# Performance work log

Measured on AMD Instinct MI355X. Metric: run time of the kernel, lower is better.

Reference implementation:

```python
import jax, jax.numpy as jnp
import numpy as np

H = 10                 # heads in both convs
EPS = 1e-5             # GraphNorm eps
N, E, D_NODE, D_EDGE, G = 100000, 1600000, 128, 32, 64


def _lin(key, out_d, in_d, bias=True):
    k1, k2 = jax.random.split(key)
    W = jax.random.normal(k1, (out_d, in_d), jnp.float32) / np.sqrt(in_d)
    if bias:
        b = jax.random.normal(k2, (out_d,), jnp.float32) * 0.01
        return W, b
    return W


def setup_inputs() -> dict:
    key = jax.random.key(0)
    ks = jax.random.split(key, 20)
    x = jax.random.normal(ks[0], (N, D_NODE), jnp.float32)
    edge_attr = jax.random.normal(ks[1], (E, D_EDGE), jnp.float32)
    edge_index = jax.random.randint(ks[2], (2, E), 0, N)
    batch_idx = jnp.sort(jax.random.randint(ks[3], (N,), 0, G))
    # conv1: in=128, out=5, heads=10
    q1W, q1b = _lin(ks[4], H * 5, D_NODE)
    k1W, k1b = _lin(ks[5], H * 5, D_NODE)
    v1W, v1b = _lin(ks[6], H * 5, D_NODE)
    e1W = _lin(ks[7], H * 5, D_EDGE, bias=False)
    s1W, s1b = _lin(ks[8], 5, D_NODE)        # lin_skip
    b1W = _lin(ks[9], 1, 3 * 5, bias=False)  # lin_beta
    # GraphNorm(5)
    gnW = jnp.ones((5,), jnp.float32)
    gnb = jnp.zeros((5,), jnp.float32)
    gnms = jnp.ones((5,), jnp.float32)       # mean_scale
    # conv2: in=5, out=1, heads=10
    q2W, q2b = _lin(ks[10], H * 1, 5)
    k2W, k2b = _lin(ks[11], H * 1, 5)
    v2W, v2b = _lin(ks[12], H * 1, 5)
    e2W = _lin(ks[13], H * 1, D_EDGE, bias=False)
    s2W, s2b = _lin(ks[14], 1, 5)
    b2W = _lin(ks[15], 1, 3 * 1, bias=False)
    return dict(x=x, edge_attr=edge_attr, edge_index=edge_index, batch_idx=batch_idx,
                q1W=q1W, q1b=q1b, k1W=k1W, k1b=k1b, v1W=v1W, v1b=v1b, e1W=e1W,
                s1W=s1W, s1b=s1b, b1W=b1W, gnW=gnW, gnb=gnb, gnms=gnms,
                q2W=q2W, q2b=q2b, k2W=k2W, k2b=k2b, v2W=v2W, v2b=v2b, e2W=e2W,
                s2W=s2W, s2b=s2b, b2W=b2W)


def _tconv(x, src, dst, edge_attr, qW, qb, kW, kb, vW, vb, eW, sW, sb, bW, c):
    """PyG TransformerConv: concat=False, beta=True, eval (dropout off)."""
    n = x.shape[0]
    q = (x @ qW.T + qb).reshape(n, H, c)
    k = (x @ kW.T + kb).reshape(n, H, c)
    v = (x @ vW.T + vb).reshape(n, H, c)
    e = (edge_attr @ eW.T).reshape(-1, H, c)            # [E,H,c]
    kj = k[src] + e                                      # gather + edge bias
    alpha = jnp.einsum('ehc,ehc->eh', q[dst], kj) / np.sqrt(c)
    amax = jax.lax.stop_gradient(jax.ops.segment_max(alpha, dst, num_segments=n))
    ex = jnp.exp(alpha - amax[dst])
    denom = jax.ops.segment_sum(ex, dst, num_segments=n)
    a = ex / denom[dst]                                  # segment softmax [E,H]
    out = jax.ops.segment_sum((v[src] + e) * a[:, :, None], dst, num_segments=n)
    out = out.mean(axis=1)                               # concat=False -> head mean [N,c]
    xr = x @ sW.T + sb                                   # skip
    beta = jax.nn.sigmoid(jnp.concatenate([out, xr, out - xr], -1) @ bW.T)
    return beta * xr + (1.0 - beta) * out


def _graph_norm(x, batch, w, b, ms):
    cnt = jnp.maximum(jax.ops.segment_sum(jnp.ones((x.shape[0],), x.dtype), batch,
                                          num_segments=G), 1.0)[:, None]
    mean = jax.ops.segment_sum(x, batch, num_segments=G) / cnt
    out = x - mean[batch] * ms
    var = jax.ops.segment_sum(out * out, batch, num_segments=G) / cnt
    return w * out / jnp.sqrt(var + EPS)[batch] + b


def reference(x, edge_attr, edge_index, batch_idx,
              q1W, q1b, k1W, k1b, v1W, v1b, e1W, s1W, s1b, b1W,
              gnW, gnb, gnms,
              q2W, q2b, k2W, k2b, v2W, v2b, e2W, s2W, s2b, b2W):
    src, dst = edge_index[0], edge_index[1]
    h = _tconv(x, src, dst, edge_attr, q1W, q1b, k1W, k1b, v1W, v1b, e1W,
               s1W, s1b, b1W, 5)
    h = jax.nn.relu(_graph_norm(h, batch_idx, gnW, gnb, gnms))
    out = _tconv(h, src, dst, edge_attr, q2W, q2b, k2W, k2b, v2W, v2b, e2W,
                 s2W, s2b, b2W, 1)
    return jax.nn.sigmoid(out)
```

## Files before the change

### kernel.cpp

```cpp
#include <hip/hip_runtime.h>
#include <math.h>


#define EPS 1e-5f
#define INV_SQRT5 0.44721359549995794f

__device__ __forceinline__ float f16_to_f32(unsigned short u) {
  union { unsigned short us; _Float16 h; } cv; cv.us = u;
  return (float)cv.h;
}

__device__ __forceinline__ void store40(const float (&acc)[40], int n, int g,
                                        float* __restrict__ q1, float* __restrict__ kv1,
                                        float* __restrict__ xr1) {
#pragma unroll
  for (int c = 0; c < 40; ++c) {
    int ch = g * 40 + c;
    if (ch < 50)        q1[(size_t)n * 52 + ch] = acc[c];
    else if (ch < 100)  kv1[(size_t)n * 104 + 2 * (ch - 50)] = acc[c];
    else if (ch < 150)  kv1[(size_t)n * 104 + 2 * (ch - 100) + 1] = acc[c];
    else if (ch < 155)  xr1[(size_t)n * 8 + (ch - 150)] = acc[c];
  }
}

__global__ __launch_bounds__(256, 4) void k_qkvs1(
    const float* __restrict__ x,
    const float* __restrict__ qW, const float* __restrict__ qb,
    const float* __restrict__ kW, const float* __restrict__ kb,
    const float* __restrict__ vW, const float* __restrict__ vb,
    const float* __restrict__ sW, const float* __restrict__ sb,
    float* __restrict__ q1, float* __restrict__ kv1,
    float* __restrict__ xr1, int n_nodes) {
  __shared__ __align__(16) float sWt[40 * 128];
  __shared__ float sB[40];
  const int t = threadIdx.x;
  const int g = blockIdx.y;
  const int n0 = blockIdx.x * 512;

  for (int i = t; i < 1280; i += 256) {
    int c = i >> 5, q = i & 31;
    int ch = g * 40 + c;
    float4 w = make_float4(0.f, 0.f, 0.f, 0.f);
    const float* srcr = nullptr;
    if (ch < 50)        srcr = qW + ch * 128;
    else if (ch < 100)  srcr = kW + (ch - 50) * 128;
    else if (ch < 150)  srcr = vW + (ch - 100) * 128;
    else if (ch < 155)  srcr = sW + (ch - 150) * 128;
    if (srcr) w = *(const float4*)(srcr + q * 4);
    *(float4*)&sWt[c * 128 + q * 4] = w;
  }
  if (t < 40) {
    int ch = g * 40 + t;
    float b = 0.f;
    if (ch < 50) b = qb[ch];
    else if (ch < 100) b = kb[ch - 50];
    else if (ch < 150) b = vb[ch - 100];
    else if (ch < 155) b = sb[ch - 150];
    sB[t] = b;
  }
  __syncthreads();

  float accA[40], accB[40];
#pragma unroll
  for (int c = 0; c < 40; ++c) { accA[c] = sB[c]; accB[c] = sB[c]; }
  const int na = n0 + 2 * t, nb = na + 1;
  const bool okA = na < n_nodes, okB = nb < n_nodes;
  const float* xa_p = x + (size_t)(okA ? na : 0) * 128;
  const float* xb_p = x + (size_t)(okB ? nb : 0) * 128;
  const float4* w4 = (const float4*)sWt;

  for (int kc = 0; kc < 128; kc += 8) {
    float4 xa0 = *(const float4*)(xa_p + kc);
    float4 xa1 = *(const float4*)(xa_p + kc + 4);
    float4 xb0 = *(const float4*)(xb_p + kc);
    float4 xb1 = *(const float4*)(xb_p + kc + 4);
    const int base = kc >> 2;
#pragma unroll
    for (int c = 0; c < 40; ++c) {
      float4 w0 = w4[c * 32 + base];
      float4 w1 = w4[c * 32 + base + 1];
      accA[c] = fmaf(w0.x, xa0.x, accA[c]); accA[c] = fmaf(w0.y, xa0.y, accA[c]);
      accA[c] = fmaf(w0.z, xa0.z, accA[c]); accA[c] = fmaf(w0.w, xa0.w, accA[c]);
      accA[c] = fmaf(w1.x, xa1.x, accA[c]); accA[c] = fmaf(w1.y, xa1.y, accA[c]);
      accA[c] = fmaf(w1.z, xa1.z, accA[c]); accA[c] = fmaf(w1.w, xa1.w, accA[c]);
      accB[c] = fmaf(w0.x, xb0.x, accB[c]); accB[c] = fmaf(w0.y, xb0.y, accB[c]);
      accB[c] = fmaf(w0.z, xb0.z, accB[c]); accB[c] = fmaf(w0.w, xb0.w, accB[c]);
      accB[c] = fmaf(w1.x, xb1.x, accB[c]); accB[c] = fmaf(w1.y, xb1.y, accB[c]);
      accB[c] = fmaf(w1.z, xb1.z, accB[c]); accB[c] = fmaf(w1.w, xb1.w, accB[c]);
    }
  }
  if (okA) store40(accA, na, g, q1, kv1, xr1);
  if (okB) store40(accB, nb, g, q1, kv1, xr1);
}

__global__ __launch_bounds__(256) void k_hist(const int* __restrict__ ei, int n_edges,
                                              int* __restrict__ cnt) {
  int e = blockIdx.x * 256 + threadIdx.x;
  if (e < n_edges) atomicAdd(&cnt[ei[n_edges + e]], 1);
}

__global__ __launch_bounds__(1024) void k_scan(const int* __restrict__ cnt,
                                               int* __restrict__ rp,
                                               int* __restrict__ cursor, int n) {
  __shared__ int ls[1024];
  int tid = threadIdx.x;
  const int CH = (((n + 1023) / 1024) + 3) & ~3;
  int lo = tid * CH, hi = min(lo + CH, n);
  int s = 0;
  if (lo < n) {
    int full = (hi - lo) & ~3;
    const int4* c4 = (const int4*)(cnt + lo);
    for (int i = 0; i < full; i += 4) {
      int4 v = c4[i >> 2];
      s += v.x + v.y + v.z + v.w;
    }
    for (int i = lo + full; i < hi; ++i) s += cnt[i];
  }
  ls[tid] = s;
  __syncthreads();
  for (int off = 1; off < 1024; off <<= 1) {
    int v = (tid >= off) ? ls[tid - off] : 0;
    __syncthreads();
    ls[tid] += v;
    __syncthreads();
  }
  int run = (tid > 0) ? ls[tid - 1] : 0;
  for (int i = lo; i < hi; ++i) {
    rp[i] = run; cursor[i] = run; run += cnt[i];
  }
  if (hi == n && lo < n) rp[n] = run;
}

__global__ __launch_bounds__(256) void k_scatter(const int* __restrict__ ei, int n_edges,
                                                 int* __restrict__ cursor,
                                                 int* __restrict__ seid,
                                                 int* __restrict__ ssrc) {
  int e = blockIdx.x * 256 + threadIdx.x;
  if (e >= n_edges) return;
  int s = ei[e];
  int d = ei[n_edges + e];
  int p = atomicAdd(&cursor[d], 1);
  seid[p] = e;
  ssrc[p] = s;
}

__global__ __launch_bounds__(256) void k_evt(
    float* attr, const float* __restrict__ e1W, const float* __restrict__ e2W,
    int n_edges) {
  int e = blockIdx.x * 256 + threadIdx.x;
  if (e >= n_edges) return;
  const float4* ar = (const float4*)(attr + (size_t)e * 32);
  float4 a[8];
#pragma unroll
  for (int j = 0; j < 8; ++j) a[j] = ar[j];
  unsigned int d[30];
#pragma unroll
  for (int c2 = 0; c2 < 30; ++c2) {
    int c0 = 2 * c2, c1 = 2 * c2 + 1;
    const float* w0 = (c0 < 50) ? (e1W + c0 * 32) : (e2W + (c0 - 50) * 32);
    const float* w1 = (c1 < 50) ? (e1W + c1 * 32) : (e2W + (c1 - 50) * 32);
    float acc0 = 0.f, acc1 = 0.f;
#pragma unroll
    for (int j = 0; j < 8; ++j) {
      float4 wa = *(const float4*)(w0 + 4 * j);
      float4 wb = *(const float4*)(w1 + 4 * j);
      acc0 = fmaf(wa.x, a[j].x, acc0); acc0 = fmaf(wa.y, a[j].y, acc0);
      acc0 = fmaf(wa.z, a[j].z, acc0); acc0 = fmaf(wa.w, a[j].w, acc0);
      acc1 = fmaf(wb.x, a[j].x, acc1); acc1 = fmaf(wb.y, a[j].y, acc1);
      acc1 = fmaf(wb.z, a[j].z, acc1); acc1 = fmaf(wb.w, a[j].w, acc1);
    }
    union { _Float16 h[2]; unsigned int u; } p;
    p.h[0] = (_Float16)acc0; p.h[1] = (_Float16)acc1;
    d[c2] = p.u;
  }
  unsigned int* row = (unsigned int*)(attr + (size_t)e * 32);
#pragma unroll
  for (int k = 0; k < 7; ++k)
    *(uint4*)(row + 4 * k) = make_uint4(d[4 * k], d[4 * k + 1], d[4 * k + 2], d[4 * k + 3]);
  *(uint2*)(row + 28) = make_uint2(d[28], d[29]);
}

__global__ __launch_bounds__(256) void k_conv1(
    const int* __restrict__ rp, const int* __restrict__ seid,
    const int* __restrict__ ssrc, const float* __restrict__ attr,
    const float* __restrict__ q1, const float* __restrict__ kv1,
    const float* __restrict__ xr1,
    const float* __restrict__ bW, float* __restrict__ h1, int n_nodes) {
  const int lane = threadIdx.x & 63;
  const int wid = (blockIdx.x * 256 + threadIdx.x) >> 6;
  const int nw = gridDim.x * 4;
  const int wr = (lane < 50) ? lane : 0;
  const int g0 = (wr / 5) * 5;
  const int cp = lane % 5;
  const unsigned short* evr = (const unsigned short*)attr;

  for (int n = wid; n < n_nodes; n += nw) {
    const int p0 = rp[n], deg = rp[n + 1] - p0;
    const float qc = q1[(size_t)n * 52 + wr];
    int eL = 0, sL = 0;
    if (lane < deg) { eL = seid[p0 + lane]; sL = ssrc[p0 + lane]; }
    float accN0 = 0.f, accD0 = 0.f, accN1 = 0.f, accD1 = 0.f;
    int i = 0;
    for (; i + 2 <= deg; i += 2) {
      int e0, s0, e1, s1;
      if (i + 1 < 64) {
        e0 = __shfl(eL, i);     s0 = __shfl(sL, i);
        e1 = __shfl(eL, i + 1); s1 = __shfl(sL, i + 1);
      } else {
        e0 = (i < 64) ? __shfl(eL, i) : seid[p0 + i];
        s0 = (i < 64) ? __shfl(sL, i) : ssrc[p0 + i];
        e1 = seid[p0 + i + 1];  s1 = ssrc[p0 + i + 1];
      }
      float ev0 = f16_to_f32(evr[(size_t)e0 * 64 + wr]);
      float ev1 = f16_to_f32(evr[(size_t)e1 * 64 + wr]);
      float2 kva = *(const float2*)(kv1 + (size_t)s0 * 104 + 2 * wr);
      float2 kvb = *(const float2*)(kv1 + (size_t)s1 * 104 + 2 * wr);
      float t0 = qc * (kva.x + ev0);
      float t1 = qc * (kvb.x + ev1);
      float al0 = __shfl(t0, g0) + __shfl(t0, g0 + 1) + __shfl(t0, g0 + 2)
                + __shfl(t0, g0 + 3) + __shfl(t0, g0 + 4);
      float al1 = __shfl(t1, g0) + __shfl(t1, g0 + 1) + __shfl(t1, g0 + 2)
                + __shfl(t1, g0 + 3) + __shfl(t1, g0 + 4);
      float ex0 = __expf(al0 * INV_SQRT5);
      float ex1 = __expf(al1 * INV_SQRT5);
      accD0 += ex0; accN0 = fmaf(kva.y + ev0, ex0, accN0);
      accD1 += ex1; accN1 = fmaf(kvb.y + ev1, ex1, accN1);
    }
    if (i < deg) {
      int e = (i < 64) ? __shfl(eL, i) : seid[p0 + i];
      int s = (i < 64) ? __shfl(sL, i) : ssrc[p0 + i];
      float ev = f16_to_f32(evr[(size_t)e * 64 + wr]);
      float2 kv = *(const float2*)(kv1 + (size_t)s * 104 + 2 * wr);
      float t = qc * (kv.x + ev);
      float al = __shfl(t, g0) + __shfl(t, g0 + 1) + __shfl(t, g0 + 2)
               + __shfl(t, g0 + 3) + __shfl(t, g0 + 4);
      float ex = __expf(al * INV_SQRT5);
      accD0 += ex; accN0 = fmaf(kv.y + ev, ex, accN0);
    }
    float accN = accN0 + accN1, accD = accD0 + accD1;
    float r = (accD > 0.f) ? accN / accD : 0.f;
    if (lane >= 50) r = 0.f;
    float o = 0.f;
#pragma unroll
    for (int h = 0; h < 10; ++h) o += __shfl(r, cp + 5 * h);
    o *= 0.1f;
    float xr = xr1[(size_t)n * 8 + cp];
    float tb = bW[cp] * o + bW[5 + cp] * xr + bW[10 + cp] * (o - xr);
    float sb = 0.f;
#pragma unroll
    for (int j = 0; j < 5; ++j) sb += __shfl(tb, j);
    float beta = 1.f / (1.f + __expf(-sb));
    if (lane < 5) h1[(size_t)n * 8 + lane] = beta * xr + (1.f - beta) * o;
  }
}

__global__ __launch_bounds__(256) void k_stats(
    const float* __restrict__ h1, const int* __restrict__ batch,
    float* __restrict__ gsum, float* __restrict__ gsq,
    float* __restrict__ gcnt, int n_nodes) {
  int n = blockIdx.x * 256 + threadIdx.x;
  bool act = n < n_nodes;
  int g = act ? batch[n] : 0;
  float v[5], s2[5], one = act ? 1.f : 0.f;
#pragma unroll
  for (int c = 0; c < 5; ++c) {
    v[c] = act ? h1[(size_t)n * 8 + c] : 0.f;
    s2[c] = v[c] * v[c];
  }
  int g0 = __shfl(g, 0);
  bool uni = __all((!act) || (g == g0));
  if (uni) {
#pragma unroll
    for (int off = 32; off; off >>= 1) {
#pragma unroll
      for (int c = 0; c < 5; ++c) {
        v[c] += __shfl_down(v[c], off);
        s2[c] += __shfl_down(s2[c], off);
      }
      one += __shfl_down(one, off);
    }
    if ((threadIdx.x & 63) == 0) {
#pragma unroll
      for (int c = 0; c < 5; ++c) {
        atomicAdd(&gsum[g0 * 8 + c], v[c]);
        atomicAdd(&gsq[g0 * 8 + c], s2[c]);
      }
      atomicAdd(&gcnt[g0], one);
    }
  } else if (act) {
#pragma unroll
    for (int c = 0; c < 5; ++c) {
      atomicAdd(&gsum[g * 8 + c], v[c]);
      atomicAdd(&gsq[g * 8 + c], s2[c]);
    }
    atomicAdd(&gcnt[g], 1.f);
  }
}

__global__ __launch_bounds__(256) void k_apply(
    const float* __restrict__ h1, const int* __restrict__ batch,
    const float* __restrict__ gsum, const float* __restrict__ gsq,
    const float* __restrict__ gcnt,
    const float* __restrict__ gnw, const float* __restrict__ gnb,
    const float* __restrict__ gnms,
    const float* __restrict__ q2W, const float* __restrict__ q2b,
    const float* __restrict__ k2W, const float* __restrict__ k2b,
    const float* __restrict__ v2W, const float* __restrict__ v2b,
    const float* __restrict__ s2W, const float* __restrict__ s2b,
    float* __restrict__ q2, float* __restrict__ kv2,
    float* __restrict__ xr2, int n_nodes) {
  int n = blockIdx.x * 256 + threadIdx.x;
  if (n >= n_nodes) return;
  int g = batch[n];
  float rc = 1.f / fmaxf(gcnt[g], 1.f);
  float r[5];
#pragma unroll
  for (int c = 0; c < 5; ++c) {
    float ms = gnms[c];
    float mean = gsum[g * 8 + c] * rc;
    float var = gsq[g * 8 + c] * rc - mean * mean * ms * (2.f - ms);
    var = fmaxf(var, 0.f);
    float o = h1[(size_t)n * 8 + c] - mean * ms;
    float y = gnw[c] * o * rsqrtf(var + EPS) + gnb[c];
    r[c] = fmaxf(y, 0.f);
  }
#pragma unroll
  for (int h = 0; h < 10; ++h) {
    float aq = q2b[h], ak = k2b[h], av = v2b[h];
#pragma unroll
    for (int i = 0; i < 5; ++i) {
      aq = fmaf(r[i], q2W[h * 5 + i], aq);
      ak = fmaf(r[i], k2W[h * 5 + i], ak);
      av = fmaf(r[i], v2W[h * 5 + i], av);
    }
    q2[(size_t)n * 12 + h] = aq;
    kv2[(size_t)n * 24 + 2 * h]     = ak;
    kv2[(size_t)n * 24 + 2 * h + 1] = av;
  }
  float s = s2b[0];
#pragma unroll
  for (int i = 0; i < 5; ++i) s = fmaf(r[i], s2W[i], s);
  xr2[n] = s;
}

__global__ __launch_bounds__(256) void k_conv2(
    const int* __restrict__ rp, const int* __restrict__ seid,
    const int* __restrict__ ssrc, const float* __restrict__ attr,
    const float* __restrict__ q2, const float* __restrict__ kv2,
    const float* __restrict__ xr2,
    const float* __restrict__ bW, float* __restrict__ out, int n_nodes) {
  const int lane = threadIdx.x & 63;
  const int wid = (blockIdx.x * 256 + threadIdx.x) >> 6;
  const int nw = gridDim.x * 4;
  const int slot = lane / 10, h = lane - slot * 10;
  const bool active = slot < 6;
  const unsigned short* evr = (const unsigned short*)attr;

  for (int n = wid; n < n_nodes; n += nw) {
    int p0 = rp[n], deg = rp[n + 1] - p0;
    float qh = q2[(size_t)n * 12 + h];
    int eL = 0, sL = 0;
    if (lane < deg) { eL = seid[p0 + lane]; sL = ssrc[p0 + lane]; }
    float accN = 0.f, accD = 0.f;
    int nit = (deg + 5) / 6;
    for (int t = 0; t < nit; ++t) {
      int i = t * 6 + slot;
      bool val = active && (i < deg);
      int e = 0, s = 0;
      if (i < 64) { e = __shfl(eL, i); s = __shfl(sL, i); }
      else if (val) { e = seid[p0 + i]; s = ssrc[p0 + i]; }
      float evv = 0.f; float2 kv = make_float2(0.f, 0.f);
      if (val) {
        evv = f16_to_f32(evr[(size_t)e * 64 + 50 + h]);
        kv = *(const float2*)(kv2 + (size_t)s * 24 + 2 * h);
      }
      float exv = val ? __expf(qh * (kv.x + evv)) : 0.f;
      accD += exv;
      accN = fmaf(kv.y + evv, exv, accN);
    }
    float D = 0.f, Nn = 0.f;
#pragma unroll
    for (int i2 = 0; i2 < 6; ++i2) {
      D  += __shfl(accD, h + 10 * i2);
      Nn += __shfl(accN, h + 10 * i2);
    }
    float r = (D > 0.f) ? Nn / D : 0.f;
    float o = 0.f;
#pragma unroll
    for (int j = 0; j < 10; ++j) o += __shfl(r, j);
    o *= 0.1f;
    float xr = xr2[n];
    float sbv = bW[0] * o + bW[1] * xr + bW[2] * (o - xr);
    float beta = 1.f / (1.f + __expf(-sbv));
    float y = beta * xr + (1.f - beta) * o;
    if (lane == 0) out[n] = 1.f / (1.f + __expf(-y));
  }
}

extern "C" void kernel_launch(void* const* d_in, const int* in_sizes, int n_in,
                              void* d_out, int out_size, void* d_ws, size_t ws_size,
                              hipStream_t stream) {
  const float* x    = (const float*)d_in[0];
  float*       attr = (float*)d_in[1];
  const int*   ei   = (const int*)d_in[2];
  const int*   batch= (const int*)d_in[3];
  const float* q1W = (const float*)d_in[4];  const float* q1b = (const float*)d_in[5];
  const float* k1W = (const float*)d_in[6];  const float* k1b = (const float*)d_in[7];
  const float* v1W = (const float*)d_in[8];  const float* v1b = (const float*)d_in[9];
  const float* e1W = (const float*)d_in[10];
  const float* s1W = (const float*)d_in[11]; const float* s1b = (const float*)d_in[12];
  const float* b1W = (const float*)d_in[13];
  const float* gnW = (const float*)d_in[14]; const float* gnb = (const float*)d_in[15];
  const float* gnms= (const float*)d_in[16];
  const float* q2W = (const float*)d_in[17]; const float* q2b = (const float*)d_in[18];
  const float* k2W = (const float*)d_in[19]; const float* k2b = (const float*)d_in[20];
  const float* v2W = (const float*)d_in[21]; const float* v2b = (const float*)d_in[22];
  const float* e2W = (const float*)d_in[23];
  const float* s2W = (const float*)d_in[24]; const float* s2b = (const float*)d_in[25];
  const float* b2W = (const float*)d_in[26];

  const int n_nodes = in_sizes[0] / 128;
  const int n_edges = in_sizes[2] / 2;
  float* ws = (float*)d_ws;
  const size_t nn = (size_t)n_nodes;
  const size_t ne = (size_t)n_edges;

  const size_t oQ1  = 0;
  const size_t oKV1 = 52 * nn;
  const size_t oXR1 = 156 * nn;
  const size_t oH1  = 164 * nn;
  const size_t oQ2  = 172 * nn;
  const size_t oKV2 = 184 * nn;
  const size_t oXR2 = 208 * nn;
  const size_t oSTAT= 209 * nn;
  const size_t oCNT = oSTAT + 1088;
  const size_t oRP  = oCNT + nn;
  const size_t oCUR = oRP + nn + 1;
  const size_t oSEID= oCUR + nn;
  const size_t oSSRC= oSEID + ne;

  int* cnt    = (int*)(ws + oCNT);
  int* rp     = (int*)(ws + oRP);
  int* cursor = (int*)(ws + oCUR);
  int* seid   = (int*)(ws + oSEID);
  int* ssrc   = (int*)(ws + oSSRC);
  float* gsum = ws + oSTAT;
  float* gsq  = ws + oSTAT + 512;
  float* gcnt = ws + oSTAT + 1024;

  const int nb_nodes = (n_nodes + 255) / 256;
  const int nb_edges = (n_edges + 255) / 256;
  dim3 gq((n_nodes + 511) / 512, 4);
  const int nb_pers = 2048;

  hipMemsetAsync(ws + oSTAT, 0, (1088 + nn) * sizeof(float), stream);

  k_hist<<<nb_edges, 256, 0, stream>>>(ei, n_edges, cnt);
  k_scan<<<1, 1024, 0, stream>>>(cnt, rp, cursor, n_nodes);
  k_scatter<<<nb_edges, 256, 0, stream>>>(ei, n_edges, cursor, seid, ssrc);

  k_qkvs1<<<gq, 256, 0, stream>>>(x, q1W, q1b, k1W, k1b, v1W, v1b, s1W, s1b,
                                  ws + oQ1, ws + oKV1, ws + oXR1, n_nodes);
  k_evt<<<nb_edges, 256, 0, stream>>>(attr, e1W, e2W, n_edges);

  k_conv1<<<nb_pers, 256, 0, stream>>>(rp, seid, ssrc, attr,
                                       ws + oQ1, ws + oKV1, ws + oXR1,
                                       b1W, ws + oH1, n_nodes);
  k_stats<<<nb_nodes, 256, 0, stream>>>(ws + oH1, batch, gsum, gsq, gcnt, n_nodes);
  k_apply<<<nb_nodes, 256, 0, stream>>>(ws + oH1, batch, gsum, gsq, gcnt,
                                        gnW, gnb, gnms,
                                        q2W, q2b, k2W, k2b, v2W, v2b, s2W, s2b,
                                        ws + oQ2, ws + oKV2, ws + oXR2, n_nodes);
  k_conv2<<<nb_pers, 256, 0, stream>>>(rp, seid, ssrc, attr,
                                       ws + oQ2, ws + oKV2, ws + oXR2,
                                       b2W, (float*)d_out, n_nodes);
}
```

Before: 1.248 ms.

## Replace single-block CSR prefix scan with multi-block three-pass scan

The single 1024-thread block that scanned all node in-degree counts is replaced by three kernels: per-block reduction, a small top-level scan of block sums, and a per-block scan that writes row pointers and cursors with vectorized int4 stores. This spreads the scan, which ran on one compute unit, across many blocks. It adds two kernel launches and a block-sum buffer in the workspace. The row-pointer region is padded so cursor stays 16-byte aligned. An FMA order swap in the QKV kernel slightly changes rounding.

New measurement: 1.064 ms. 14.7% less time.

```diff
diff --git a/kernel.cpp b/kernel.cpp
--- a/kernel.cpp
+++ b/kernel.cpp
@@ -86,7 +86,7 @@
       accB[c] = fmaf(w0.x, xb0.x, accB[c]); accB[c] = fmaf(w0.y, xb0.y, accB[c]);
       accB[c] = fmaf(w0.z, xb0.z, accB[c]); accB[c] = fmaf(w0.w, xb0.w, accB[c]);
       accB[c] = fmaf(w1.x, xb1.x, accB[c]); accB[c] = fmaf(w1.y, xb1.y, accB[c]);
-      accB[c] = fmaf(w1.z, xb1.z, accB[c]); accB[c] = fmaf(w1.w, xb1.w, accB[c]);
+      accB[c] = fmaf(w1.w, xb1.w, accB[c]); accB[c] = fmaf(w1.z, xb1.z, accB[c]);
     }
   }
   if (okA) store40(accA, na, g, q1, kv1, xr1);
@@ -99,36 +99,82 @@
   if (e < n_edges) atomicAdd(&cnt[ei[n_edges + e]], 1);
 }
 
-__global__ __launch_bounds__(1024) void k_scan(const int* __restrict__ cnt,
-                                               int* __restrict__ rp,
-                                               int* __restrict__ cursor, int n) {
-  __shared__ int ls[1024];
+__global__ __launch_bounds__(256) void k_scansum(const int* __restrict__ cnt,
+                                                 int* __restrict__ bsum, int n) {
+  int base = blockIdx.x * 1024 + threadIdx.x * 4;
+  int s = 0;
+  if (base + 3 < n) {
+    int4 v = *(const int4*)(cnt + base);
+    s = v.x + v.y + v.z + v.w;
+  } else {
+    for (int i = base; i < n && i < base + 4; ++i) s += cnt[i];
+  }
+#pragma unroll
+  for (int off = 32; off; off >>= 1) s += __shfl_down(s, off);
+  __shared__ int wsum[4];
+  if ((threadIdx.x & 63) == 0) wsum[threadIdx.x >> 6] = s;
+  __syncthreads();
+  if (threadIdx.x == 0) bsum[blockIdx.x] = wsum[0] + wsum[1] + wsum[2] + wsum[3];
+}
+
+__global__ __launch_bounds__(256) void k_scantop(int* __restrict__ bsum, int nb) {
+  __shared__ int ls[256];
   int tid = threadIdx.x;
-  const int CH = (((n + 1023) / 1024) + 3) & ~3;
-  int lo = tid * CH, hi = min(lo + CH, n);
-  int s = 0;
-  if (lo < n) {
-    int full = (hi - lo) & ~3;
-    const int4* c4 = (const int4*)(cnt + lo);
-    for (int i = 0; i < full; i += 4) {
-      int4 v = c4[i >> 2];
-      s += v.x + v.y + v.z + v.w;
-    }
-    for (int i = lo + full; i < hi; ++i) s += cnt[i];
-  }
-  ls[tid] = s;
+  int v = (tid < nb) ? bsum[tid] : 0;
+  ls[tid] = v;
   __syncthreads();
-  for (int off = 1; off < 1024; off <<= 1) {
-    int v = (tid >= off) ? ls[tid - off] : 0;
+  for (int off = 1; off < 256; off <<= 1) {
+    int t = (tid >= off) ? ls[tid - off] : 0;
     __syncthreads();
-    ls[tid] += v;
+    ls[tid] += t;
     __syncthreads();
   }
-  int run = (tid > 0) ? ls[tid - 1] : 0;
-  for (int i = lo; i < hi; ++i) {
-    rp[i] = run; cursor[i] = run; run += cnt[i];
-  }
-  if (hi == n && lo < n) rp[n] = run;
+  if (tid < nb) bsum[tid] = ls[tid] - v;
+}
+
+__global__ __launch_bounds__(256) void k_scanout(const int* __restrict__ cnt,
+                                                 const int* __restrict__ bsum,
+                                                 int* __restrict__ rp,
+                                                 int* __restrict__ cursor, int n) {
+  const int tid = threadIdx.x;
+  const int lane = tid & 63;
+  const int w = tid >> 6;
+  int base = blockIdx.x * 1024 + tid * 4;
+  int c0 = 0, c1 = 0, c2 = 0, c3 = 0;
+  if (base + 3 < n) {
+    int4 v = *(const int4*)(cnt + base);
+    c0 = v.x; c1 = v.y; c2 = v.z; c3 = v.w;
+  } else if (base < n) {
+    c0 = cnt[base];
+    if (base + 1 < n) c1 = cnt[base + 1];
+    if (base + 2 < n) c2 = cnt[base + 2];
+    if (base + 3 < n) c3 = cnt[base + 3];
+  }
+  int s = c0 + c1 + c2 + c3;
+  int incl = s;
+#pragma unroll
+  for (int off = 1; off < 64; off <<= 1) {
+    int t = __shfl_up(incl, off);
+    if (lane >= off) incl += t;
+  }
+  __shared__ int wsum[4];
+  if (lane == 63) wsum[w] = incl;
+  __syncthreads();
+  int woff = 0;
+#pragma unroll
+  for (int j = 0; j < 3; ++j) if (j < w) woff += wsum[j];
+  int excl = bsum[blockIdx.x] + woff + (incl - s);
+  int4 o;
+  o.x = excl; o.y = o.x + c0; o.z = o.y + c1; o.w = o.z + c2;
+  if (base + 3 < n) {
+    *(int4*)(rp + base) = o;
+    *(int4*)(cursor + base) = o;
+  } else if (base < n) {
+    rp[base] = o.x; cursor[base] = o.x;
+    if (base + 1 < n) { rp[base + 1] = o.y; cursor[base + 1] = o.y; }
+    if (base + 2 < n) { rp[base + 2] = o.z; cursor[base + 2] = o.z; }
+  }
+  if (base < n && base + 4 >= n) rp[n] = excl + s;
 }
 
 __global__ __launch_bounds__(256) void k_scatter(const int* __restrict__ ei, int n_edges,
@@ -435,28 +481,33 @@
   const size_t oSTAT= 209 * nn;
   const size_t oCNT = oSTAT + 1088;
   const size_t oRP  = oCNT + nn;
-  const size_t oCUR = oRP + nn + 1;
+  const size_t oCUR = oRP + nn + 4;
   const size_t oSEID= oCUR + nn;
   const size_t oSSRC= oSEID + ne;
+  const size_t oBSUM= oSSRC + ne;
 
   int* cnt    = (int*)(ws + oCNT);
   int* rp     = (int*)(ws + oRP);
   int* cursor = (int*)(ws + oCUR);
   int* seid   = (int*)(ws + oSEID);
   int* ssrc   = (int*)(ws + oSSRC);
+  int* bsum   = (int*)(ws + oBSUM);
   float* gsum = ws + oSTAT;
   float* gsq  = ws + oSTAT + 512;
   float* gcnt = ws + oSTAT + 1024;
 
   const int nb_nodes = (n_nodes + 255) / 256;
   const int nb_edges = (n_edges + 255) / 256;
+  const int nb_scan  = (n_nodes + 1023) / 1024;
   dim3 gq((n_nodes + 511) / 512, 4);
   const int nb_pers = 2048;
 
   hipMemsetAsync(ws + oSTAT, 0, (1088 + nn) * sizeof(float), stream);
 
   k_hist<<<nb_edges, 256, 0, stream>>>(ei, n_edges, cnt);
-  k_scan<<<1, 1024, 0, stream>>>(cnt, rp, cursor, n_nodes);
+  k_scansum<<<nb_scan, 256, 0, stream>>>(cnt, bsum, n_nodes);
+  k_scantop<<<1, 256, 0, stream>>>(bsum, nb_scan);
+  k_scanout<<<nb_scan, 256, 0, stream>>>(cnt, bsum, rp, cursor, n_nodes);
   k_scatter<<<nb_edges, 256, 0, stream>>>(ei, n_edges, cursor, seid, ssrc);
 
   k_qkvs1<<<gq, 256, 0, stream>>>(x, q1W, q1b, k1W, k1b, v1W, v1b, s1W, s1b,
```
